# Kernel optimization log

Hardware: AMD Instinct MI355X
Metric: run time of the kernel (lower is better)

## Reference

```python
import jax, jax.numpy as jnp
import numpy as np

PULL_W = 0.1
PUSH_W = 0.1
OFF_W = 1.0
EPS = 1e-4


def _trans_output(idx, pred):
    # pred: [B, ch, H, W] -> [B, H*W, ch]; gather rows at idx [B, K]
    B, ch, H, W = pred.shape
    p = pred.transpose(0, 2, 3, 1).reshape(B, H * W, ch)
    K = idx.shape[1]
    ix = jnp.broadcast_to(idx[:, :, None], (B, K, ch))
    return jnp.take_along_axis(p, ix, axis=1)  # [B, K, ch]


def _focal_loss(t, p, alpha=2, beta=4):
    # t, p: [B, C, H, W]; p already sigmoid-ed, in (0,1)
    pos = t == 1.0
    neg = t < 1.0
    axes = (1, 2, 3)
    pos_loss = jnp.sum(jnp.where(pos, (1.0 - p) ** alpha * jnp.log(p), 0.0), axis=axes)
    neg_loss = jnp.sum(jnp.where(neg, (1.0 - t) ** beta * p ** alpha * jnp.log(1.0 - p), 0.0), axis=axes)
    n = jnp.sum(pos.astype(t.dtype), axis=axes)
    per = jnp.where(n == 0, neg_loss, (pos_loss + neg_loss) / jnp.where(n == 0, 1.0, n))
    return -jnp.sum(per)


def _smooth_l1_sum(pred, true):
    d = pred - true
    ad = jnp.abs(d)
    return jnp.where(ad < 1.0, 0.5 * d * d, ad - 0.5)


def _offset_loss(true, pred, mask_f):
    # true, pred: [B, K, 2]; mask_f: [B, K] float 0/1
    num = mask_f.sum() * 2.0
    l = _smooth_l1_sum(pred, true) * mask_f[:, :, None]
    return l.sum() / (num + EPS)


def _triplet_loss(tl, br, mask_f):
    # tl, br: [B, K, 1] -> [B, K]; mask_f: [B, K]
    tl = tl[..., 0]
    br = br[..., 0]
    num = mask_f.sum(axis=1)  # [B]
    ek = (tl + br) / 2.0
    inv = 1.0 / (num[:, None] + EPS)
    pull = jnp.sum(((tl - ek) ** 2 + (br - ek) ** 2) * inv * mask_f)

    pair_mask = (mask_f[:, :, None] + mask_f[:, None, :]) == 2.0  # [B, K, K]
    num_b = num[:, None, None]
    num2 = (num_b - 1.0) * num_b
    m = 2.0
    dist = ek[:, None, :] - ek[:, :, None]  # matches ek.unsqueeze(1) - ek.unsqueeze(2)
    dist = jax.nn.relu(m - jnp.abs(dist))
    dist = dist - m / (num_b + EPS)
    dist = dist / (num2 + EPS)
    push = jnp.sum(jnp.where(pair_mask, dist, 0.0))
    return pull, push


def _cornernet_loss(true_tl_heat, true_br_heat, true_tl_off, true_br_off,
                    pred_tl_heat, pred_br_heat, pred_tl_off, pred_br_off,
                    pred_tl_emb, pred_br_emb, idx_tl, idx_br, mask):
    mask_f = mask.astype(jnp.float32)
    p_tl = jax.nn.sigmoid(pred_tl_heat)
    p_br = jax.nn.sigmoid(pred_br_heat)
    det_loss = 0.5 * (_focal_loss(true_tl_heat, p_tl) + _focal_loss(true_br_heat, p_br))

    ptl_off = _trans_output(idx_tl, pred_tl_off)
    pbr_off = _trans_output(idx_br, pred_br_off)
    off_loss = OFF_W * _offset_loss(true_tl_off, ptl_off, mask_f) + OFF_W * _offset_loss(true_br_off, pbr_off, mask_f)

    tl_e = _trans_output(idx_tl, pred_tl_emb)
    br_e = _trans_output(idx_br, pred_br_emb)
    pull, push = _triplet_loss(tl_e, br_e, mask_f)

    B = true_tl_heat.shape[0]
    loss = (det_loss + pull + push + off_loss) / B
    return loss


def setup_inputs() -> dict:
    key = jax.random.key(0)
    ks = jax.random.split(key, 16)
    B, C, H, W = 16, 80, 128, 128
    K = 128
    t_tl = jax.random.uniform(ks[0], (B, C, H, W), dtype=jnp.float32)
    t_tl = jnp.where(t_tl > 0.998, 1.0, t_tl)  # sparse exact-1 corner peaks
    t_br = jax.random.uniform(ks[1], (B, C, H, W), dtype=jnp.float32)
    t_br = jnp.where(t_br > 0.998, 1.0, t_br)
    return {
        "true_tl_heat": t_tl,
        "true_br_heat": t_br,
        "true_tl_off": jax.random.uniform(ks[2], (B, K, 2), dtype=jnp.float32),
        "true_br_off": jax.random.uniform(ks[3], (B, K, 2), dtype=jnp.float32),
        "pred_tl_heat": jax.random.normal(ks[4], (B, C, H, W), dtype=jnp.float32),
        "pred_br_heat": jax.random.normal(ks[5], (B, C, H, W), dtype=jnp.float32),
        "pred_tl_off": jax.random.normal(ks[6], (B, 2, H, W), dtype=jnp.float32),
        "pred_br_off": jax.random.normal(ks[7], (B, 2, H, W), dtype=jnp.float32),
        "pred_tl_emb": jax.random.normal(ks[8], (B, 1, H, W), dtype=jnp.float32),
        "pred_br_emb": jax.random.normal(ks[9], (B, 1, H, W), dtype=jnp.float32),
        "idx_tl": jax.random.randint(ks[10], (B, K), 0, H * W, dtype=jnp.int64) if jax.config.jax_enable_x64 else jax.random.randint(ks[10], (B, K), 0, H * W).astype(jnp.int32),
        "idx_br": jax.random.randint(ks[11], (B, K), 0, H * W).astype(jnp.int32),
        "mask": jax.random.randint(ks[12], (B, K), 0, 2).astype(jnp.int32),
    }


def reference(true_tl_heat, true_br_heat, true_tl_off, true_br_off,
              pred_tl_heat, pred_br_heat, pred_tl_off, pred_br_off,
              pred_tl_emb, pred_br_emb, idx_tl, idx_br, mask):
    return _cornernet_loss(true_tl_heat, true_br_heat, true_tl_off, true_br_off,
                           pred_tl_heat, pred_br_heat, pred_tl_off, pred_br_off,
                           pred_tl_emb, pred_br_emb, idx_tl, idx_br, mask)
```

## Files before the change

### kernel.cpp

```cpp
#include <hip/hip_runtime.h>
#include <math.h>

#define BB 16
#define CC 80
#define HH 128
#define WW 128
#define HW (HH*WW)
#define N1 (CC*HW)
#define KK 128
#define FEPS 1e-4f
#define FB2 64
#define NITER 20


typedef __attribute__((address_space(3))) void        as3_void;
typedef const __attribute__((address_space(1))) void  as1_void;

__device__ __forceinline__ void dma16(const void* g, void* l) {
    __builtin_amdgcn_global_load_lds((as1_void*)g, (as3_void*)l, 16, 0, 0);
}

__device__ __forceinline__ void proc(float tt, float xx,
                                     float& A, float& B, float& cnt)
{
    const float NLOG2E = -1.4426950408889634f;
    float z  = xx * NLOG2E;
    float e  = exp2f(z);
    float s  = 1.0f + e;
    float L  = __log2f(s);
    float p  = __builtin_amdgcn_rcpf(s);
    float ep = e * p;
    float a  = ep * ep * L;
    float u  = 1.0f - tt;
    float u2 = u * u;
    float pw = p * u2;
    float bv = pw * pw * (L - z);
    B += bv;
    bool pos = (tt == 1.0f);
    A   += pos ? a : 0.0f;
    cnt += pos ? 1.0f : 0.0f;
}

__global__ __launch_bounds__(256, 8) void focal_kernel(
    const float* __restrict__ t_tl, const float* __restrict__ t_br,
    const float* __restrict__ x_tl, const float* __restrict__ x_br,
    float* __restrict__ ws)
{
    const int m = blockIdx.z;
    const int b = blockIdx.y;
    const float4* __restrict__ T4 =
        (const float4*)((m ? t_br : t_tl) + (size_t)b * N1) + blockIdx.x * (NITER*256);
    const float4* __restrict__ X4 =
        (const float4*)((m ? x_br : x_tl) + (size_t)b * N1) + blockIdx.x * (NITER*256);

    __shared__ float4 sm[2][2][256];
    const int lane = threadIdx.x & 63, wv = threadIdx.x >> 6;
    const int widx = wv * 64 + lane;

    #define STAGE(slot, j) do {                                            \
        dma16((const void*)(T4 + (j)*256 + widx), (void*)&sm[slot][0][wv*64]); \
        dma16((const void*)(X4 + (j)*256 + widx), (void*)&sm[slot][1][wv*64]); \
    } while (0)

    STAGE(0, 0);
    STAGE(1, 1);

    float A = 0.0f, B = 0.0f, cnt = 0.0f;
    for (int j = 0; j < NITER; ++j) {
        const int slot = j & 1;
        if (j < NITER - 1) { asm volatile("s_waitcnt vmcnt(2)" ::: "memory"); }
        else               { asm volatile("s_waitcnt vmcnt(0)" ::: "memory"); }
        __builtin_amdgcn_sched_barrier(0);
        float4 tv = sm[slot][0][widx];
        float4 xv = sm[slot][1][widx];
        #pragma unroll
        for (int c = 0; c < 4; ++c) proc((&tv.x)[c], (&xv.x)[c], A, B, cnt);
        if (j + 2 < NITER) STAGE(slot, j + 2);
    }

    #pragma unroll
    for (int off = 32; off > 0; off >>= 1) {
        A   += __shfl_down(A  , off, 64);
        B   += __shfl_down(B  , off, 64);
        cnt += __shfl_down(cnt, off, 64);
    }
    __shared__ float red[3][4];
    if (lane == 0) { red[0][wv] = A; red[1][wv] = B; red[2][wv] = cnt; }
    __syncthreads();
    if (threadIdx.x == 0) {
        atomicAdd(&ws[m*48 +  0 + b], red[0][0] + red[0][1] + red[0][2] + red[0][3]);
        atomicAdd(&ws[m*48 + 16 + b], red[1][0] + red[1][1] + red[1][2] + red[1][3]);
        atomicAdd(&ws[m*48 + 32 + b], red[2][0] + red[2][1] + red[2][2] + red[2][3]);
    }
}

__global__ void small_kernel(
    const float* __restrict__ to_tl, const float* __restrict__ to_br,
    const float* __restrict__ po_tl, const float* __restrict__ po_br,
    const float* __restrict__ e_tl,  const float* __restrict__ e_br,
    const int* __restrict__ idx_tl,  const int* __restrict__ idx_br,
    const int* __restrict__ mask,    float* __restrict__ ws,
    float* __restrict__ out)
{
    const int b = blockIdx.x, k = threadIdx.x;
    const int lane = threadIdx.x & 63, wv = threadIdx.x >> 6;

    float mf = (float)mask[b*KK + k];
    const int itl = idx_tl[b*KK + k];
    const int ibr = idx_br[b*KK + k];

    float s_tl = 0.0f, s_br = 0.0f;
    #pragma unroll
    for (int ch = 0; ch < 2; ++ch) {
        float pv = po_tl[((size_t)b*2 + ch)*HW + itl];
        float tv = to_tl[(b*KK + k)*2 + ch];
        float d = pv - tv, ad = fabsf(d);
        s_tl += (ad < 1.0f) ? 0.5f*d*d : (ad - 0.5f);
        pv = po_br[((size_t)b*2 + ch)*HW + ibr];
        tv = to_br[(b*KK + k)*2 + ch];
        d = pv - tv; ad = fabsf(d);
        s_br += (ad < 1.0f) ? 0.5f*d*d : (ad - 0.5f);
    }
    s_tl *= mf; s_br *= mf;

    __shared__ float ek_s[KK], mf_s[KK], nred[2];
    float tl = e_tl[(size_t)b*HW + itl];
    float br = e_br[(size_t)b*HW + ibr];
    float ek = 0.5f * (tl + br);
    ek_s[k] = ek; mf_s[k] = mf;

    float nm = mf;
    #pragma unroll
    for (int off = 32; off > 0; off >>= 1) nm += __shfl_down(nm, off, 64);
    if (lane == 0) nred[wv] = nm;
    __syncthreads();
    const float num  = nred[0] + nred[1];
    const float inv  = 1.0f / (num + FEPS);
    const float num2 = (num - 1.0f) * num;
    const float inv2 = 1.0f / (num2 + FEPS);

    float pull = ((tl-ek)*(tl-ek) + (br-ek)*(br-ek)) * inv * mf;

    float push = 0.0f;
    if (mf == 1.0f) {
        for (int j = 0; j < KK; ++j) {
            if (mf_s[j] == 1.0f) {
                float d = fabsf(ek_s[j] - ek);
                push += (fmaxf(2.0f - d, 0.0f) - 2.0f * inv) * inv2;
            }
        }
    }

    #pragma unroll
    for (int off = 32; off > 0; off >>= 1) {
        s_tl += __shfl_down(s_tl, off, 64);
        s_br += __shfl_down(s_br, off, 64);
        mf   += __shfl_down(mf  , off, 64);
        pull += __shfl_down(pull, off, 64);
        push += __shfl_down(push, off, 64);
    }
    __shared__ float r[5][2];
    __shared__ int last_flag;
    if (lane == 0) {
        r[0][wv] = s_tl; r[1][wv] = s_br; r[2][wv] = mf;
        r[3][wv] = pull; r[4][wv] = push;
    }
    __syncthreads();
    if (threadIdx.x == 0) {
        atomicAdd(&ws[96],  r[0][0] + r[0][1]);
        atomicAdd(&ws[97],  r[1][0] + r[1][1]);
        atomicAdd(&ws[98],  r[2][0] + r[2][1]);
        atomicAdd(&ws[99],  r[3][0] + r[3][1]);
        atomicAdd(&ws[100], r[4][0] + r[4][1]);
        __threadfence();
        unsigned old = atomicAdd((unsigned*)&ws[104], 1u);
        last_flag = (old == BB - 1) ? 1 : 0;
    }
    __syncthreads();

    if (last_flag) {
        __shared__ float wsv[101];
        if (k < 101) wsv[k] = atomicAdd(&ws[k], 0.0f);
        __syncthreads();
        if (threadIdx.x == 0) {
            const float NLN2 = -0.6931471805599453f;
            float det = 0.0f;
            for (int m = 0; m < 2; ++m) {
                float f = 0.0f;
                for (int bb = 0; bb < BB; ++bb) {
                    float pos = NLN2 * wsv[m*48 +  0 + bb];
                    float neg = NLN2 * wsv[m*48 + 16 + bb];
                    float n   = wsv[m*48 + 32 + bb];
                    float per = (n == 0.0f) ? neg : (pos + neg) / n;
                    f -= per;
                }
                det += 0.5f * f;
            }
            float numoff = wsv[98] * 2.0f;
            float off = wsv[96] / (numoff + FEPS) + wsv[97] / (numoff + FEPS);
            out[0] = (det + wsv[99] + wsv[100] + off) / (float)BB;
        }
    }
}

extern "C" void kernel_launch(void* const* d_in, const int* in_sizes, int n_in,
                              void* d_out, int out_size, void* d_ws, size_t ws_size,
                              hipStream_t stream) {
    const float* t_tl  = (const float*)d_in[0];
    const float* t_br  = (const float*)d_in[1];
    const float* to_tl = (const float*)d_in[2];
    const float* to_br = (const float*)d_in[3];
    const float* x_tl  = (const float*)d_in[4];
    const float* x_br  = (const float*)d_in[5];
    const float* po_tl = (const float*)d_in[6];
    const float* po_br = (const float*)d_in[7];
    const float* e_tl  = (const float*)d_in[8];
    const float* e_br  = (const float*)d_in[9];
    const int* idx_tl  = (const int*)d_in[10];
    const int* idx_br  = (const int*)d_in[11];
    const int* mask    = (const int*)d_in[12];
    float* ws = (float*)d_ws;

    hipMemsetAsync(ws, 0, 512, stream);
    focal_kernel<<<dim3(FB2, BB, 2), 256, 0, stream>>>(t_tl, t_br, x_tl, x_br, ws);
    small_kernel<<<BB, KK, 0, stream>>>(to_tl, to_br, po_tl, po_br, e_tl, e_br,
                                        idx_tl, idx_br, mask, ws, (float*)d_out);
}
```

Baseline: 95.65 us.

## Fuse focal and small kernels into one launch with register prefetch pipeline

Merges the focal-loss streaming kernel and the small offset/embedding kernel into a single launch. The last finishing block, picked with an atomic counter over all blocks, does the final reduction, so the second kernel launch and its gap disappear. The focal path also drops the global-to-LDS DMA double-buffering in favour of a fully unrolled register prefetch three iterations deep. This raises register pressure under the 256x8 launch bound, and the small blocks now use 256 threads with half of them idle.

```diff
diff --git a/kernel.cpp b/kernel.cpp
--- a/kernel.cpp
+++ b/kernel.cpp
@@ -3,22 +3,16 @@
 
 #define BB 16
 #define CC 80
-#define HH 128
-#define WW 128
-#define HW (HH*WW)
+#define HW (128*128)
 #define N1 (CC*HW)
 #define KK 128
 #define FEPS 1e-4f
 #define FB2 64
 #define NITER 20
-
-
-typedef __attribute__((address_space(3))) void        as3_void;
-typedef const __attribute__((address_space(1))) void  as1_void;
-
-__device__ __forceinline__ void dma16(const void* g, void* l) {
-    __builtin_amdgcn_global_load_lds((as1_void*)g, (as3_void*)l, 16, 0, 0);
-}
+#define NFOCAL (FB2*BB*2)
+#define NTOT (NFOCAL + BB)
+#define PFD 3
+
 
 __device__ __forceinline__ void proc(float tt, float xx,
                                      float& A, float& B, float& cnt)
@@ -41,148 +35,154 @@
     cnt += pos ? 1.0f : 0.0f;
 }
 
-__global__ __launch_bounds__(256, 8) void focal_kernel(
+__global__ __launch_bounds__(256, 8) void fused_kernel(
     const float* __restrict__ t_tl, const float* __restrict__ t_br,
     const float* __restrict__ x_tl, const float* __restrict__ x_br,
-    float* __restrict__ ws)
-{
-    const int m = blockIdx.z;
-    const int b = blockIdx.y;
-    const float4* __restrict__ T4 =
-        (const float4*)((m ? t_br : t_tl) + (size_t)b * N1) + blockIdx.x * (NITER*256);
-    const float4* __restrict__ X4 =
-        (const float4*)((m ? x_br : x_tl) + (size_t)b * N1) + blockIdx.x * (NITER*256);
-
-    __shared__ float4 sm[2][2][256];
-    const int lane = threadIdx.x & 63, wv = threadIdx.x >> 6;
-    const int widx = wv * 64 + lane;
-
-    #define STAGE(slot, j) do {                                            \
-        dma16((const void*)(T4 + (j)*256 + widx), (void*)&sm[slot][0][wv*64]); \
-        dma16((const void*)(X4 + (j)*256 + widx), (void*)&sm[slot][1][wv*64]); \
-    } while (0)
-
-    STAGE(0, 0);
-    STAGE(1, 1);
-
-    float A = 0.0f, B = 0.0f, cnt = 0.0f;
-    for (int j = 0; j < NITER; ++j) {
-        const int slot = j & 1;
-        if (j < NITER - 1) { asm volatile("s_waitcnt vmcnt(2)" ::: "memory"); }
-        else               { asm volatile("s_waitcnt vmcnt(0)" ::: "memory"); }
-        __builtin_amdgcn_sched_barrier(0);
-        float4 tv = sm[slot][0][widx];
-        float4 xv = sm[slot][1][widx];
-        #pragma unroll
-        for (int c = 0; c < 4; ++c) proc((&tv.x)[c], (&xv.x)[c], A, B, cnt);
-        if (j + 2 < NITER) STAGE(slot, j + 2);
-    }
-
-    #pragma unroll
-    for (int off = 32; off > 0; off >>= 1) {
-        A   += __shfl_down(A  , off, 64);
-        B   += __shfl_down(B  , off, 64);
-        cnt += __shfl_down(cnt, off, 64);
-    }
-    __shared__ float red[3][4];
-    if (lane == 0) { red[0][wv] = A; red[1][wv] = B; red[2][wv] = cnt; }
-    __syncthreads();
-    if (threadIdx.x == 0) {
-        atomicAdd(&ws[m*48 +  0 + b], red[0][0] + red[0][1] + red[0][2] + red[0][3]);
-        atomicAdd(&ws[m*48 + 16 + b], red[1][0] + red[1][1] + red[1][2] + red[1][3]);
-        atomicAdd(&ws[m*48 + 32 + b], red[2][0] + red[2][1] + red[2][2] + red[2][3]);
-    }
-}
-
-__global__ void small_kernel(
     const float* __restrict__ to_tl, const float* __restrict__ to_br,
     const float* __restrict__ po_tl, const float* __restrict__ po_br,
     const float* __restrict__ e_tl,  const float* __restrict__ e_br,
     const int* __restrict__ idx_tl,  const int* __restrict__ idx_br,
-    const int* __restrict__ mask,    float* __restrict__ ws,
-    float* __restrict__ out)
+    const int* __restrict__ mask,
+    float* __restrict__ ws, float* __restrict__ out)
 {
-    const int b = blockIdx.x, k = threadIdx.x;
-    const int lane = threadIdx.x & 63, wv = threadIdx.x >> 6;
-
-    float mf = (float)mask[b*KK + k];
-    const int itl = idx_tl[b*KK + k];
-    const int ibr = idx_br[b*KK + k];
-
-    float s_tl = 0.0f, s_br = 0.0f;
-    #pragma unroll
-    for (int ch = 0; ch < 2; ++ch) {
-        float pv = po_tl[((size_t)b*2 + ch)*HW + itl];
-        float tv = to_tl[(b*KK + k)*2 + ch];
-        float d = pv - tv, ad = fabsf(d);
-        s_tl += (ad < 1.0f) ? 0.5f*d*d : (ad - 0.5f);
-        pv = po_br[((size_t)b*2 + ch)*HW + ibr];
-        tv = to_br[(b*KK + k)*2 + ch];
-        d = pv - tv; ad = fabsf(d);
-        s_br += (ad < 1.0f) ? 0.5f*d*d : (ad - 0.5f);
+    __shared__ float red[5][4];
+    __shared__ float ek_s[KK], mf_s[KK];
+    __shared__ float wsv[101];
+    __shared__ int last_flag;
+
+    const int tid  = threadIdx.x;
+    const int lane = tid & 63, wv = tid >> 6;
+
+    if (blockIdx.x < NFOCAL) {
+        const int bid   = blockIdx.x;
+        const int m     = bid >> 10;
+        const int r     = bid & 1023;
+        const int b     = r >> 6;
+        const int chunk = r & 63;
+        const float4* __restrict__ T4 =
+            (const float4*)((m ? t_br : t_tl) + (size_t)b * N1) + chunk * (NITER*256) + tid;
+        const float4* __restrict__ X4 =
+            (const float4*)((m ? x_br : x_tl) + (size_t)b * N1) + chunk * (NITER*256) + tid;
+
+        float4 tb0 = T4[0];       float4 xb0 = X4[0];
+        float4 tb1 = T4[256];     float4 xb1 = X4[256];
+        float4 tb2 = T4[512];     float4 xb2 = X4[512];
+        __builtin_amdgcn_sched_barrier(0);
+
+        float A = 0.0f, B = 0.0f, cnt = 0.0f;
+        #pragma unroll
+        for (int j = 0; j < NITER; ++j) {
+            float4 tn, xn;
+            if (j + PFD < NITER) {
+                tn = T4[(j + PFD) * 256];
+                xn = X4[(j + PFD) * 256];
+            }
+            __builtin_amdgcn_sched_barrier(0);
+            #pragma unroll
+            for (int c = 0; c < 4; ++c) proc((&tb0.x)[c], (&xb0.x)[c], A, B, cnt);
+            tb0 = tb1; xb0 = xb1;
+            tb1 = tb2; xb1 = xb2;
+            tb2 = tn;  xb2 = xn;
+        }
+
+        #pragma unroll
+        for (int off = 32; off > 0; off >>= 1) {
+            A   += __shfl_down(A  , off, 64);
+            B   += __shfl_down(B  , off, 64);
+            cnt += __shfl_down(cnt, off, 64);
+        }
+        if (lane == 0) { red[0][wv] = A; red[1][wv] = B; red[2][wv] = cnt; }
+        __syncthreads();
+        if (tid == 0) {
+            atomicAdd(&ws[m*48 +  0 + b], red[0][0] + red[0][1] + red[0][2] + red[0][3]);
+            atomicAdd(&ws[m*48 + 16 + b], red[1][0] + red[1][1] + red[1][2] + red[1][3]);
+            atomicAdd(&ws[m*48 + 32 + b], red[2][0] + red[2][1] + red[2][2] + red[2][3]);
+            __threadfence();
+            unsigned old = atomicAdd((unsigned*)&ws[104], 1u);
+            last_flag = (old == NTOT - 1) ? 1 : 0;
+        }
+        __syncthreads();
+    } else {
+        const int b  = blockIdx.x - NFOCAL;
+        const int kk = (tid < KK) ? tid : 0;
+        const float on = (tid < KK) ? 1.0f : 0.0f;
+
+        float mf = on * (float)mask[b*KK + kk];
+        const int itl = idx_tl[b*KK + kk];
+        const int ibr = idx_br[b*KK + kk];
+
+        float s_tl = 0.0f, s_br = 0.0f;
+        #pragma unroll
+        for (int ch = 0; ch < 2; ++ch) {
+            float pv = po_tl[((size_t)b*2 + ch)*HW + itl];
+            float tv = to_tl[(b*KK + kk)*2 + ch];
+            float d = pv - tv, ad = fabsf(d);
+            s_tl += (ad < 1.0f) ? 0.5f*d*d : (ad - 0.5f);
+            pv = po_br[((size_t)b*2 + ch)*HW + ibr];
+            tv = to_br[(b*KK + kk)*2 + ch];
+            d = pv - tv; ad = fabsf(d);
+            s_br += (ad < 1.0f) ? 0.5f*d*d : (ad - 0.5f);
+        }
+        s_tl *= mf; s_br *= mf;
+
+        float tl = e_tl[(size_t)b*HW + itl];
+        float br = e_br[(size_t)b*HW + ibr];
+        float ek = 0.5f * (tl + br);
+        if (tid < KK) { ek_s[tid] = ek; mf_s[tid] = mf; }
+
+        float nm = mf;
+        #pragma unroll
+        for (int off = 32; off > 0; off >>= 1) nm += __shfl_down(nm, off, 64);
+        if (lane == 0) red[0][wv] = nm;
+        __syncthreads();
+        const float num  = red[0][0] + red[0][1] + red[0][2] + red[0][3];
+        const float inv  = 1.0f / (num + FEPS);
+        const float num2 = (num - 1.0f) * num;
+        const float inv2 = 1.0f / (num2 + FEPS);
+
+        float pull = ((tl-ek)*(tl-ek) + (br-ek)*(br-ek)) * inv * mf;
+
+        float push = 0.0f;
+        if (mf == 1.0f) {
+            for (int j = 0; j < KK; ++j) {
+                if (mf_s[j] == 1.0f) {
+                    float d = fabsf(ek_s[j] - ek);
+                    push += (fmaxf(2.0f - d, 0.0f) - 2.0f * inv) * inv2;
+                }
+            }
+        }
+        __syncthreads();
+
+        #pragma unroll
+        for (int off = 32; off > 0; off >>= 1) {
+            s_tl += __shfl_down(s_tl, off, 64);
+            s_br += __shfl_down(s_br, off, 64);
+            mf   += __shfl_down(mf  , off, 64);
+            pull += __shfl_down(pull, off, 64);
+            push += __shfl_down(push, off, 64);
+        }
+        if (lane == 0) {
+            red[0][wv] = s_tl; red[1][wv] = s_br; red[2][wv] = mf;
+            red[3][wv] = pull; red[4][wv] = push;
+        }
+        __syncthreads();
+        if (tid == 0) {
+            atomicAdd(&ws[96],  red[0][0] + red[0][1] + red[0][2] + red[0][3]);
+            atomicAdd(&ws[97],  red[1][0] + red[1][1] + red[1][2] + red[1][3]);
+            atomicAdd(&ws[98],  red[2][0] + red[2][1] + red[2][2] + red[2][3]);
+            atomicAdd(&ws[99],  red[3][0] + red[3][1] + red[3][2] + red[3][3]);
+            atomicAdd(&ws[100], red[4][0] + red[4][1] + red[4][2] + red[4][3]);
+            __threadfence();
+            unsigned old = atomicAdd((unsigned*)&ws[104], 1u);
+            last_flag = (old == NTOT - 1) ? 1 : 0;
+        }
+        __syncthreads();
     }
-    s_tl *= mf; s_br *= mf;
-
-    __shared__ float ek_s[KK], mf_s[KK], nred[2];
-    float tl = e_tl[(size_t)b*HW + itl];
-    float br = e_br[(size_t)b*HW + ibr];
-    float ek = 0.5f * (tl + br);
-    ek_s[k] = ek; mf_s[k] = mf;
-
-    float nm = mf;
-    #pragma unroll
-    for (int off = 32; off > 0; off >>= 1) nm += __shfl_down(nm, off, 64);
-    if (lane == 0) nred[wv] = nm;
-    __syncthreads();
-    const float num  = nred[0] + nred[1];
-    const float inv  = 1.0f / (num + FEPS);
-    const float num2 = (num - 1.0f) * num;
-    const float inv2 = 1.0f / (num2 + FEPS);
-
-    float pull = ((tl-ek)*(tl-ek) + (br-ek)*(br-ek)) * inv * mf;
-
-    float push = 0.0f;
-    if (mf == 1.0f) {
-        for (int j = 0; j < KK; ++j) {
-            if (mf_s[j] == 1.0f) {
-                float d = fabsf(ek_s[j] - ek);
-                push += (fmaxf(2.0f - d, 0.0f) - 2.0f * inv) * inv2;
-            }
-        }
-    }
-
-    #pragma unroll
-    for (int off = 32; off > 0; off >>= 1) {
-        s_tl += __shfl_down(s_tl, off, 64);
-        s_br += __shfl_down(s_br, off, 64);
-        mf   += __shfl_down(mf  , off, 64);
-        pull += __shfl_down(pull, off, 64);
-        push += __shfl_down(push, off, 64);
-    }
-    __shared__ float r[5][2];
-    __shared__ int last_flag;
-    if (lane == 0) {
-        r[0][wv] = s_tl; r[1][wv] = s_br; r[2][wv] = mf;
-        r[3][wv] = pull; r[4][wv] = push;
-    }
-    __syncthreads();
-    if (threadIdx.x == 0) {
-        atomicAdd(&ws[96],  r[0][0] + r[0][1]);
-        atomicAdd(&ws[97],  r[1][0] + r[1][1]);
-        atomicAdd(&ws[98],  r[2][0] + r[2][1]);
-        atomicAdd(&ws[99],  r[3][0] + r[3][1]);
-        atomicAdd(&ws[100], r[4][0] + r[4][1]);
-        __threadfence();
-        unsigned old = atomicAdd((unsigned*)&ws[104], 1u);
-        last_flag = (old == BB - 1) ? 1 : 0;
-    }
-    __syncthreads();
 
     if (last_flag) {
-        __shared__ float wsv[101];
-        if (k < 101) wsv[k] = atomicAdd(&ws[k], 0.0f);
-        __syncthreads();
-        if (threadIdx.x == 0) {
+        if (tid < 101) wsv[tid] = atomicAdd(&ws[tid], 0.0f);
+        __syncthreads();
+        if (tid == 0) {
             const float NLN2 = -0.6931471805599453f;
             float det = 0.0f;
             for (int m = 0; m < 2; ++m) {
@@ -222,7 +222,8 @@
     float* ws = (float*)d_ws;
 
     hipMemsetAsync(ws, 0, 512, stream);
-    focal_kernel<<<dim3(FB2, BB, 2), 256, 0, stream>>>(t_tl, t_br, x_tl, x_br, ws);
-    small_kernel<<<BB, KK, 0, stream>>>(to_tl, to_br, po_tl, po_br, e_tl, e_br,
-                                        idx_tl, idx_br, mask, ws, (float*)d_out);
+    fused_kernel<<<NTOT, 256, 0, stream>>>(t_tl, t_br, x_tl, x_br,
+                                           to_tl, to_br, po_tl, po_br,
+                                           e_tl, e_br, idx_tl, idx_br, mask,
+                                           ws, (float*)d_out);
 }
```

Result: slower. 174.5 us (+82.4%).

## Replace LDS DMA staging with register-prefetched nontemporal loads in focal kernel

Applied to the files above, without the earlier changes.

The focal kernel stops using global_load_lds DMA into double-buffered shared memory with manual waitcnt. Each thread now issues nontemporal float4 loads straight into registers, prefetching the next iteration's two float4 pairs while computing the current ones. Each block now reads an interleaved stride across the whole grid instead of a contiguous chunk, and launch bounds are relaxed from 8 to 4 blocks per CU. This cuts LDS traffic and synchronization, but raises register pressure and may lower occupancy on what is a bandwidth-bound stream.

```diff
diff --git a/kernel.cpp b/kernel.cpp
--- a/kernel.cpp
+++ b/kernel.cpp
@@ -3,22 +3,15 @@
 
 #define BB 16
 #define CC 80
-#define HH 128
-#define WW 128
-#define HW (HH*WW)
+#define HW (128*128)
 #define N1 (CC*HW)
 #define KK 128
 #define FEPS 1e-4f
 #define FB2 64
-#define NITER 20
-
-
-typedef __attribute__((address_space(3))) void        as3_void;
-typedef const __attribute__((address_space(1))) void  as1_void;
-
-__device__ __forceinline__ void dma16(const void* g, void* l) {
-    __builtin_amdgcn_global_load_lds((as1_void*)g, (as3_void*)l, 16, 0, 0);
-}
+#define NJ 10
+
+typedef float f4 __attribute__((ext_vector_type(4)));
+
 
 __device__ __forceinline__ void proc(float tt, float xx,
                                      float& A, float& B, float& cnt)
@@ -41,41 +34,40 @@
     cnt += pos ? 1.0f : 0.0f;
 }
 
-__global__ __launch_bounds__(256, 8) void focal_kernel(
+__global__ __launch_bounds__(256, 4) void focal_kernel(
     const float* __restrict__ t_tl, const float* __restrict__ t_br,
     const float* __restrict__ x_tl, const float* __restrict__ x_br,
     float* __restrict__ ws)
 {
     const int m = blockIdx.z;
     const int b = blockIdx.y;
-    const float4* __restrict__ T4 =
-        (const float4*)((m ? t_br : t_tl) + (size_t)b * N1) + blockIdx.x * (NITER*256);
-    const float4* __restrict__ X4 =
-        (const float4*)((m ? x_br : x_tl) + (size_t)b * N1) + blockIdx.x * (NITER*256);
-
-    __shared__ float4 sm[2][2][256];
-    const int lane = threadIdx.x & 63, wv = threadIdx.x >> 6;
-    const int widx = wv * 64 + lane;
-
-    #define STAGE(slot, j) do {                                            \
-        dma16((const void*)(T4 + (j)*256 + widx), (void*)&sm[slot][0][wv*64]); \
-        dma16((const void*)(X4 + (j)*256 + widx), (void*)&sm[slot][1][wv*64]); \
-    } while (0)
-
-    STAGE(0, 0);
-    STAGE(1, 1);
+    const f4* __restrict__ T4 = (const f4*)((m ? t_br : t_tl) + (size_t)b * N1);
+    const f4* __restrict__ X4 = (const f4*)((m ? x_br : x_tl) + (size_t)b * N1);
+
+    const int JS = FB2 * 512;
+    const int p0 = blockIdx.x * 512 + threadIdx.x;
+
+    f4 ct0 = __builtin_nontemporal_load(T4 + p0);
+    f4 cx0 = __builtin_nontemporal_load(X4 + p0);
+    f4 ct1 = __builtin_nontemporal_load(T4 + p0 + 256);
+    f4 cx1 = __builtin_nontemporal_load(X4 + p0 + 256);
 
     float A = 0.0f, B = 0.0f, cnt = 0.0f;
-    for (int j = 0; j < NITER; ++j) {
-        const int slot = j & 1;
-        if (j < NITER - 1) { asm volatile("s_waitcnt vmcnt(2)" ::: "memory"); }
-        else               { asm volatile("s_waitcnt vmcnt(0)" ::: "memory"); }
-        __builtin_amdgcn_sched_barrier(0);
-        float4 tv = sm[slot][0][widx];
-        float4 xv = sm[slot][1][widx];
+    #pragma unroll
+    for (int j = 0; j < NJ; ++j) {
+        f4 nt0, nx0, nt1, nx1;
+        if (j + 1 < NJ) {
+            const int q = p0 + (j + 1) * JS;
+            nt0 = __builtin_nontemporal_load(T4 + q);
+            nx0 = __builtin_nontemporal_load(X4 + q);
+            nt1 = __builtin_nontemporal_load(T4 + q + 256);
+            nx1 = __builtin_nontemporal_load(X4 + q + 256);
+        }
         #pragma unroll
-        for (int c = 0; c < 4; ++c) proc((&tv.x)[c], (&xv.x)[c], A, B, cnt);
-        if (j + 2 < NITER) STAGE(slot, j + 2);
+        for (int c = 0; c < 4; ++c) proc(ct0[c], cx0[c], A, B, cnt);
+        #pragma unroll
+        for (int c = 0; c < 4; ++c) proc(ct1[c], cx1[c], A, B, cnt);
+        ct0 = nt0; cx0 = nx0; ct1 = nt1; cx1 = nx1;
     }
 
     #pragma unroll
@@ -85,6 +77,7 @@
         cnt += __shfl_down(cnt, off, 64);
     }
     __shared__ float red[3][4];
+    const int lane = threadIdx.x & 63, wv = threadIdx.x >> 6;
     if (lane == 0) { red[0][wv] = A; red[1][wv] = B; red[2][wv] = cnt; }
     __syncthreads();
     if (threadIdx.x == 0) {
@@ -221,7 +214,7 @@
     const int* mask    = (const int*)d_in[12];
     float* ws = (float*)d_ws;
 
-    hipMemsetAsync(ws, 0, 512, stream);
+    (void)hipMemsetAsync(ws, 0, 512, stream);
     focal_kernel<<<dim3(FB2, BB, 2), 256, 0, stream>>>(t_tl, t_br, x_tl, x_br, ws);
     small_kernel<<<BB, KK, 0, stream>>>(to_tl, to_br, po_tl, po_br, e_tl, e_br,
                                         idx_tl, idx_br, mask, ws, (float*)d_out);
```

After: 84.29 us. 1.13x faster.
